# Kernel tuning notes

Measured on AMD Instinct MI355X. Metric: run time of the kernel, lower is better.

The kernel has to match this reference:

```python
import jax, jax.numpy as jnp
import numpy as np

ENTREG = 0.1          # blur passed to geomloss SamplesLoss
P_EXP = 2             # p=2 -> squared euclidean cost
EPS = ENTREG ** P_EXP # geomloss temperature eps = blur**p = 0.01
N_ITERS = 30          # fixed Sinkhorn iterations (geomloss tensorized loop)


def _squared_distances(x, y):
    # C[i,j] = ||x_i - y_j||^2  (geomloss.utils.squared_distances)
    x2 = jnp.sum(x * x, axis=-1)  # [n]
    y2 = jnp.sum(y * y, axis=-1)  # [m]
    return x2[:, None] + y2[None, :] - 2.0 * (x @ y.T)


def setup_inputs() -> dict:
    key = jax.random.key(0)
    k1, k2 = jax.random.split(key)
    Xs = jax.random.normal(k1, (4096, 1024), dtype=jnp.float32)
    Xt = jax.random.normal(k2, (4096, 1024), dtype=jnp.float32)
    return {"Xs": Xs, "Xt": Xt}


def _sinkhorn_plan(Xs, Xt):
    n, m = Xs.shape[0], Xt.shape[0]
    C = _squared_distances(Xs, Xt)          # [n, m]
    loga = -jnp.log(jnp.float32(n))         # uniform source weights (log)
    logb = -jnp.log(jnp.float32(m))         # uniform target weights (log)
    f0 = jnp.zeros((n,), dtype=C.dtype)
    g0 = jnp.zeros((m,), dtype=C.dtype)

    def step(carry, _):
        f, g = carry
        # softmin updates in log-domain (stable logsumexp), eps = blur**p
        g = -EPS * jax.nn.logsumexp((f[:, None] - C) / EPS + loga, axis=0)  # [m]
        f = -EPS * jax.nn.logsumexp((g[None, :] - C) / EPS + logb, axis=1)  # [n]
        return (f, g), None

    (f, g), _ = jax.lax.scan(jax.checkpoint(step), (f0, g0), None, length=N_ITERS)
    # closs: P = exp((u^T + v - C) / entreg)  -- note: entreg, not eps, as in source
    P = jnp.exp((f[:, None] + g[None, :] - C) / ENTREG)
    return P


def reference(Xs, Xt):
    return _sinkhorn_plan(Xs, Xt)
```

## Files before the change

### kernel.cpp

```cpp
#include <hip/hip_runtime.h>
#include <cstddef>
#include <cstdint>

#define N_PTS 4096
#define DIMK 1024

typedef _Float16 half8 __attribute__((ext_vector_type(8)));
typedef float floatx4 __attribute__((ext_vector_type(4)));

static constexpr float S_SCALE = 144.26950408889634f;
static constexpr float TWO_S   = 288.53900817779268f;
static constexpr float NEG_BIG = -3.4e38f;


__device__ __forceinline__ float4 f4max(float4 a, float4 b) {
  return make_float4(fmaxf(a.x, b.x), fmaxf(a.y, b.y), fmaxf(a.z, b.z), fmaxf(a.w, b.w));
}
__device__ __forceinline__ void msmerge(float4& M, float4& S, const float4 M2, const float4 S2) {
  float4 Mn = f4max(M, M2);
  S.x = S.x * exp2f(M.x - Mn.x) + S2.x * exp2f(M2.x - Mn.x);
  S.y = S.y * exp2f(M.y - Mn.y) + S2.y * exp2f(M2.y - Mn.y);
  S.z = S.z * exp2f(M.z - Mn.z) + S2.z * exp2f(M2.z - Mn.z);
  S.w = S.w * exp2f(M.w - Mn.w) + S2.w * exp2f(M2.w - Mn.w);
  M = Mn;
}

__global__ __launch_bounds__(256) void k_prep(const float* __restrict__ Xs,
                                              float* __restrict__ fvec) {
  int row  = blockIdx.x * 4 + (threadIdx.x >> 6);
  int lane = threadIdx.x & 63;
  const float* src = Xs + (size_t)row * DIMK;
  float s = 0.f;
#pragma unroll
  for (int r = 0; r < 4; ++r) {
    float4 a = *(const float4*)(src + lane * 4 + r * 256);
    s += a.x * a.x + a.y * a.y + a.z * a.z + a.w * a.w;
  }
#pragma unroll
  for (int off = 32; off; off >>= 1) s += __shfl_xor(s, off);
  if (lane == 0) fvec[row] = (1024.0f - s) * S_SCALE;
}

__global__ __launch_bounds__(256) void k_convert(const float* __restrict__ X,
                                                 _Float16* __restrict__ H,
                                                 _Float16* __restrict__ L) {
  size_t i8 = ((size_t)blockIdx.x * 256 + threadIdx.x) * 8;
  float4 a = *(const float4*)(X + i8);
  float4 b = *(const float4*)(X + i8 + 4);
  float v[8] = {a.x, a.y, a.z, a.w, b.x, b.y, b.z, b.w};
  half8 h, l;
#pragma unroll
  for (int q = 0; q < 8; ++q) {
    _Float16 hh = (_Float16)v[q];
    h[q] = hh;
    l[q] = (_Float16)(v[q] - (float)hh);
  }
  *(half8*)(H + i8) = h;
  *(half8*)(L + i8) = l;
}

__global__ __launch_bounds__(256) void k_gemm_mfma(const _Float16* __restrict__ Ah,
                                                   const _Float16* __restrict__ Al,
                                                   const _Float16* __restrict__ Bh,
                                                   const _Float16* __restrict__ Bl,
                                                   float* __restrict__ D,
                                                   float* __restrict__ DT) {
  __shared__ __align__(16) _Float16 Ahs[128 * 32];
  __shared__ __align__(16) _Float16 Als[128 * 32];
  __shared__ __align__(16) _Float16 Bhs[128 * 32];
  __shared__ __align__(16) _Float16 Bls[128 * 32];
  const int t    = threadIdx.x;
  const int lane = t & 63, wave = t >> 6;
  const int wm = wave >> 1, wn = wave & 1;
  const int lm = lane & 15, q = lane >> 4;
  const int row0 = blockIdx.y * 128, col0 = blockIdx.x * 128;

  floatx4 acc[4][4];
#pragma unroll
  for (int i = 0; i < 4; ++i)
#pragma unroll
    for (int j = 0; j < 4; ++j) acc[i][j] = (floatx4){0.f, 0.f, 0.f, 0.f};

  const int r0 = t >> 2, p0 = t & 3;
  const int r1 = 64 + r0;

  for (int k0 = 0; k0 < DIMK; k0 += 32) {
    size_t ga0 = (size_t)(row0 + r0) * DIMK + k0 + p0 * 8;
    size_t ga1 = (size_t)(row0 + r1) * DIMK + k0 + p0 * 8;
    size_t gb0 = (size_t)(col0 + r0) * DIMK + k0 + p0 * 8;
    size_t gb1 = (size_t)(col0 + r1) * DIMK + k0 + p0 * 8;
    half8 vah0 = *(const half8*)(Ah + ga0);
    half8 vah1 = *(const half8*)(Ah + ga1);
    half8 val0 = *(const half8*)(Al + ga0);
    half8 val1 = *(const half8*)(Al + ga1);
    half8 vbh0 = *(const half8*)(Bh + gb0);
    half8 vbh1 = *(const half8*)(Bh + gb1);
    half8 vbl0 = *(const half8*)(Bl + gb0);
    half8 vbl1 = *(const half8*)(Bl + gb1);
    __syncthreads();
    ((half8*)Ahs)[t] = vah0; ((half8*)Ahs)[t + 256] = vah1;
    ((half8*)Als)[t] = val0; ((half8*)Als)[t + 256] = val1;
    ((half8*)Bhs)[t] = vbh0; ((half8*)Bhs)[t + 256] = vbh1;
    ((half8*)Bls)[t] = vbl0; ((half8*)Bls)[t + 256] = vbl1;
    __syncthreads();

    half8 afh[4], afl[4], bfh[4], bfl[4];
#pragma unroll
    for (int i = 0; i < 4; ++i) {
      int ar = (wm * 64 + i * 16 + lm) * 32 + q * 8;
      int br = (wn * 64 + i * 16 + lm) * 32 + q * 8;
      afh[i] = *(const half8*)(Ahs + ar);
      afl[i] = *(const half8*)(Als + ar);
      bfh[i] = *(const half8*)(Bhs + br);
      bfl[i] = *(const half8*)(Bls + br);
    }
#pragma unroll
    for (int i = 0; i < 4; ++i)
#pragma unroll
      for (int j = 0; j < 4; ++j) {
        acc[i][j] = __builtin_amdgcn_mfma_f32_16x16x32_f16(afh[i], bfh[j], acc[i][j], 0, 0, 0);
        acc[i][j] = __builtin_amdgcn_mfma_f32_16x16x32_f16(afh[i], bfl[j], acc[i][j], 0, 0, 0);
        acc[i][j] = __builtin_amdgcn_mfma_f32_16x16x32_f16(afl[i], bfh[j], acc[i][j], 0, 0, 0);
      }
  }

#pragma unroll
  for (int i = 0; i < 4; ++i) {
    int mbase = row0 + wm * 64 + i * 16 + q * 4;
#pragma unroll
    for (int j = 0; j < 4; ++j) {
      int n = col0 + wn * 64 + j * 16 + lm;
      float vals[4];
#pragma unroll
      for (int r = 0; r < 4; ++r) {
        float vv = -TWO_S * acc[i][j][r];
        vals[r] = vv;
        D[(size_t)(mbase + r) * N_PTS + n] = vv;
      }
      if (DT) *(float4*)(DT + (size_t)n * N_PTS + mbase) = *(float4*)vals;
    }
  }
}

__global__ __launch_bounds__(256) void k_sweep2(const float* __restrict__ Mrow,
                                                const float* __restrict__ vin,
                                                float* __restrict__ vout) {
  __shared__ float vs[N_PTS];
  const int t = threadIdx.x;
  const int l = t & 63;
  const int row = blockIdx.x * 4 + (t >> 6);
#pragma unroll
  for (int k = 0; k < 4; ++k)
    *(float4*)(vs + t * 4 + k * 1024) = *(const float4*)(vin + t * 4 + k * 1024);
  __syncthreads();
  const float* rp_ = Mrow + (size_t)row * N_PTS;
  float4 dv[16];
#pragma unroll
  for (int k = 0; k < 16; ++k) dv[k] = *(const float4*)(rp_ + l * 4 + k * 256);
  float M = NEG_BIG, S = 0.f;
#pragma unroll
  for (int c = 0; c < 4; ++c) {
    float v[16];
#pragma unroll
    for (int q = 0; q < 4; ++q) {
      float4 d = dv[c * 4 + q];
      const float* gp = vs + l * 4 + (c * 4 + q) * 256;
      v[q * 4 + 0] = gp[0] - d.x; v[q * 4 + 1] = gp[1] - d.y;
      v[q * 4 + 2] = gp[2] - d.z; v[q * 4 + 3] = gp[3] - d.w;
    }
    float Mc = v[0];
#pragma unroll
    for (int q = 1; q < 16; ++q) Mc = fmaxf(Mc, v[q]);
    float Mn = fmaxf(M, Mc);
    float s = S * exp2f(M - Mn);
#pragma unroll
    for (int q = 0; q < 16; ++q) s += exp2f(v[q] - Mn);
    M = Mn; S = s;
  }
#pragma unroll
  for (int off = 32; off; off >>= 1) {
    float M2 = __shfl_xor(M, off);
    float S2 = __shfl_xor(S, off);
    float Mn = fmaxf(M, M2);
    S = S * exp2f(M - Mn) + S2 * exp2f(M2 - Mn);
    M = Mn;
  }
  if (l == 0) vout[row] = 12.0f - M - log2f(S);
}

__global__ __launch_bounds__(256) void k_sweepF(float* __restrict__ D,
                                                const float* __restrict__ gvec) {
  __shared__ float vs[N_PTS];
  const int t = threadIdx.x;
  const int l = t & 63;
  const int row = blockIdx.x * 4 + (t >> 6);
#pragma unroll
  for (int k = 0; k < 4; ++k)
    *(float4*)(vs + t * 4 + k * 1024) = *(const float4*)(gvec + t * 4 + k * 1024);
  __syncthreads();
  float* rp_ = D + (size_t)row * N_PTS;
  float4 dv[16];
#pragma unroll
  for (int k = 0; k < 16; ++k) dv[k] = *(const float4*)(rp_ + l * 4 + k * 256);
  float M = NEG_BIG, S = 0.f;
#pragma unroll
  for (int c = 0; c < 4; ++c) {
    float v[16];
#pragma unroll
    for (int q = 0; q < 4; ++q) {
      float4 d = dv[c * 4 + q];
      const float* gp = vs + l * 4 + (c * 4 + q) * 256;
      v[q * 4 + 0] = gp[0] - d.x; v[q * 4 + 1] = gp[1] - d.y;
      v[q * 4 + 2] = gp[2] - d.z; v[q * 4 + 3] = gp[3] - d.w;
    }
    float Mc = v[0];
#pragma unroll
    for (int q = 1; q < 16; ++q) Mc = fmaxf(Mc, v[q]);
    float Mn = fmaxf(M, Mc);
    float s = S * exp2f(M - Mn);
#pragma unroll
    for (int q = 0; q < 16; ++q) s += exp2f(v[q] - Mn);
    M = Mn; S = s;
  }
#pragma unroll
  for (int off = 32; off; off >>= 1) {
    float M2 = __shfl_xor(M, off);
    float S2 = __shfl_xor(S, off);
    float Mn = fmaxf(M, M2);
    S = S * exp2f(M - Mn) + S2 * exp2f(M2 - Mn);
    M = Mn;
  }
  const float fi = 12.0f - M - log2f(S);
#pragma unroll
  for (int k = 0; k < 16; ++k) {
    int j = l * 4 + k * 256;
    float4 d = dv[k];
    const float* gp = vs + j;
    d.x = exp2f(0.1f * (fi + gp[0] - d.x));
    d.y = exp2f(0.1f * (fi + gp[1] - d.y));
    d.z = exp2f(0.1f * (fi + gp[2] - d.z));
    d.w = exp2f(0.1f * (fi + gp[3] - d.w));
    *(float4*)(rp_ + j) = d;
  }
}

__device__ __forceinline__ float lse_row4096(const float* __restrict__ rowp,
                                             const float* __restrict__ vin,
                                             int l) {
  float4 dv[16], gv[16];
#pragma unroll
  for (int k = 0; k < 16; ++k) dv[k] = *(const float4*)(rowp + l * 4 + k * 256);
#pragma unroll
  for (int k = 0; k < 16; ++k) gv[k] = *(const float4*)(vin + l * 4 + k * 256);
  float M = NEG_BIG, S = 0.f;
#pragma unroll
  for (int c = 0; c < 4; ++c) {
    float v[16];
#pragma unroll
    for (int q = 0; q < 4; ++q) {
      float4 d = dv[c * 4 + q], g = gv[c * 4 + q];
      v[q * 4 + 0] = g.x - d.x; v[q * 4 + 1] = g.y - d.y;
      v[q * 4 + 2] = g.z - d.z; v[q * 4 + 3] = g.w - d.w;
    }
    float Mc = v[0];
#pragma unroll
    for (int q = 1; q < 16; ++q) Mc = fmaxf(Mc, v[q]);
    float Mn = fmaxf(M, Mc);
    float s = S * exp2f(M - Mn);
#pragma unroll
    for (int q = 0; q < 16; ++q) s += exp2f(v[q] - Mn);
    M = Mn; S = s;
  }
#pragma unroll
  for (int off = 32; off; off >>= 1) {
    float M2 = __shfl_xor(M, off);
    float S2 = __shfl_xor(S, off);
    float Mn = fmaxf(M, M2);
    S = S * exp2f(M - Mn) + S2 * exp2f(M2 - Mn);
    M = Mn;
  }
  return 12.0f - M - log2f(S);
}

__global__ __launch_bounds__(256) void k_sweep(const float* __restrict__ Mrow,
                                               const float* __restrict__ vin,
                                               float* __restrict__ vout) {
  const int l = threadIdx.x & 63;
  const int row = blockIdx.x * 4 + (threadIdx.x >> 6);
  float r = lse_row4096(Mrow + (size_t)row * N_PTS, vin, l);
  if (l == 0) vout[row] = r;
}

__global__ __launch_bounds__(1024) void k_colpass(const float* __restrict__ D,
                                                  const float* __restrict__ fvec,
                                                  float* __restrict__ gvec) {
  __shared__ float fs[N_PTS];
  __shared__ float4 MS[16][4][2];
  const int t = threadIdx.x;
  *(float4*)(fs + t * 4) = *(const float4*)(fvec + t * 4);
  __syncthreads();
  const int c4 = t & 3;
  const int rp = t >> 2;
  const float* base = D + blockIdx.x * 16 + c4 * 4;
  float4 M = make_float4(NEG_BIG, NEG_BIG, NEG_BIG, NEG_BIG);
  float4 S = make_float4(0.f, 0.f, 0.f, 0.f);
#pragma unroll
  for (int h = 0; h < 2; ++h) {
    float4 v[8];
#pragma unroll
    for (int qq = 0; qq < 8; ++qq) {
      int r = rp + (h * 8 + qq) * 256;
      float4 d = *(const float4*)(base + (size_t)r * N_PTS);
      float fr = fs[r];
      v[qq] = make_float4(fr - d.x, fr - d.y, fr - d.z, fr - d.w);
    }
    float4 Mc = f4max(f4max(f4max(v[0], v[1]), f4max(v[2], v[3])),
                      f4max(f4max(v[4], v[5]), f4max(v[6], v[7])));
    float4 Mn = f4max(M, Mc);
    float4 s;
    s.x = S.x * exp2f(M.x - Mn.x);
    s.y = S.y * exp2f(M.y - Mn.y);
    s.z = S.z * exp2f(M.z - Mn.z);
    s.w = S.w * exp2f(M.w - Mn.w);
#pragma unroll
    for (int qq = 0; qq < 8; ++qq) {
      s.x += exp2f(v[qq].x - Mn.x);
      s.y += exp2f(v[qq].y - Mn.y);
      s.z += exp2f(v[qq].z - Mn.z);
      s.w += exp2f(v[qq].w - Mn.w);
    }
    M = Mn; S = s;
  }
#pragma unroll
  for (int off = 4; off <= 32; off <<= 1) {
    float4 M2, S2;
    M2.x = __shfl_xor(M.x, off); M2.y = __shfl_xor(M.y, off);
    M2.z = __shfl_xor(M.z, off); M2.w = __shfl_xor(M.w, off);
    S2.x = __shfl_xor(S.x, off); S2.y = __shfl_xor(S.y, off);
    S2.z = __shfl_xor(S.z, off); S2.w = __shfl_xor(S.w, off);
    msmerge(M, S, M2, S2);
  }
  const int wv = t >> 6, l = t & 63;
  if (l < 4) { MS[wv][l][0] = M; MS[wv][l][1] = S; }
  __syncthreads();
  if (t < 4) {
    float4 M0 = MS[0][t][0], S0 = MS[0][t][1];
#pragma unroll
    for (int w = 1; w < 16; ++w) msmerge(M0, S0, MS[w][t][0], MS[w][t][1]);
    float4 g;
    g.x = 12.0f - M0.x - log2f(S0.x);
    g.y = 12.0f - M0.y - log2f(S0.y);
    g.z = 12.0f - M0.z - log2f(S0.z);
    g.w = 12.0f - M0.w - log2f(S0.w);
    *(float4*)(gvec + blockIdx.x * 16 + t * 4) = g;
  }
}

__global__ __launch_bounds__(256) void k_final(float* __restrict__ D,
                                               const float* __restrict__ fvec,
                                               const float* __restrict__ gvec) {
  size_t idx = ((size_t)blockIdx.x * 256 + threadIdx.x) * 8;
  int i = (int)(idx >> 12);
  int j = (int)(idx & (N_PTS - 1));
  float fi = fvec[i];
#pragma unroll
  for (int h = 0; h < 2; ++h) {
    float4 d  = *(float4*)(D + idx + h * 4);
    float4 g4 = *(const float4*)(gvec + j + h * 4);
    d.x = exp2f(0.1f * (fi + g4.x - d.x));
    d.y = exp2f(0.1f * (fi + g4.y - d.y));
    d.z = exp2f(0.1f * (fi + g4.z - d.z));
    d.w = exp2f(0.1f * (fi + g4.w - d.w));
    *(float4*)(D + idx + h * 4) = d;
  }
}

__global__ __launch_bounds__(256) void k_gemm(const float* __restrict__ A,
                                              const float* __restrict__ B,
                                              float* __restrict__ D) {
  __shared__ float As[16][132];
  __shared__ float Bs[16][132];
  const int t  = threadIdx.x;
  const int tx = t & 15, ty = t >> 4;
  const int row0 = blockIdx.y * 128, col0 = blockIdx.x * 128;
  float acc[8][8];
#pragma unroll
  for (int i = 0; i < 8; ++i)
#pragma unroll
    for (int j = 0; j < 8; ++j) acc[i][j] = 0.f;
  for (int k0 = 0; k0 < DIMK; k0 += 16) {
#pragma unroll
    for (int s2 = 0; s2 < 2; ++s2) {
      int f4i = t + s2 * 256;
      int r   = f4i >> 2;
      int kp  = (f4i & 3) << 2;
      float4 a4 = *(const float4*)(A + (size_t)(row0 + r) * DIMK + k0 + kp);
      float4 b4 = *(const float4*)(B + (size_t)(col0 + r) * DIMK + k0 + kp);
      As[kp + 0][r] = a4.x; As[kp + 1][r] = a4.y; As[kp + 2][r] = a4.z; As[kp + 3][r] = a4.w;
      Bs[kp + 0][r] = b4.x; Bs[kp + 1][r] = b4.y; Bs[kp + 2][r] = b4.z; Bs[kp + 3][r] = b4.w;
    }
    __syncthreads();
#pragma unroll
    for (int kk = 0; kk < 16; ++kk) {
      float a[8], b[8];
      *(float4*)(a)     = *(const float4*)(&As[kk][ty * 4]);
      *(float4*)(a + 4) = *(const float4*)(&As[kk][64 + ty * 4]);
      *(float4*)(b)     = *(const float4*)(&Bs[kk][tx * 4]);
      *(float4*)(b + 4) = *(const float4*)(&Bs[kk][64 + tx * 4]);
#pragma unroll
      for (int i = 0; i < 8; ++i)
#pragma unroll
        for (int j = 0; j < 8; ++j) acc[i][j] = fmaf(a[i], b[j], acc[i][j]);
    }
    __syncthreads();
  }
#pragma unroll
  for (int i = 0; i < 8; ++i) {
    int r = row0 + ((i < 4) ? (ty * 4 + i) : (64 + ty * 4 + (i - 4)));
    float* out = D + (size_t)r * N_PTS + col0;
    float4 o1, o2;
    o1.x = -TWO_S * acc[i][0]; o1.y = -TWO_S * acc[i][1];
    o1.z = -TWO_S * acc[i][2]; o1.w = -TWO_S * acc[i][3];
    o2.x = -TWO_S * acc[i][4]; o2.y = -TWO_S * acc[i][5];
    o2.z = -TWO_S * acc[i][6]; o2.w = -TWO_S * acc[i][7];
    *(float4*)(out + tx * 4)      = o1;
    *(float4*)(out + 64 + tx * 4) = o2;
  }
}

extern "C" void kernel_launch(void* const* d_in, const int* in_sizes, int n_in,
                              void* d_out, int out_size, void* d_ws, size_t ws_size,
                              hipStream_t stream) {
  const float* Xs = (const float*)d_in[0];
  const float* Xt = (const float*)d_in[1];
  float* D   = (float*)d_out;
  char* wsb  = (char*)d_ws;
  float* fvec = (float*)wsb;
  float* gvec = fvec + N_PTS;

  const size_t halfElems = (size_t)N_PTS * DIMK;
  const size_t offHalves = 32768;
  _Float16* Ah = (_Float16*)(wsb + offHalves);
  _Float16* Al = Ah + halfElems;
  _Float16* Bh = Al + halfElems;
  _Float16* Bl = Bh + halfElems;
  float* DT = (float*)(wsb + offHalves + 4 * halfElems * sizeof(_Float16));
  const size_t needHalves = offHalves + 4 * halfElems * sizeof(_Float16);
  const size_t needFull   = needHalves + (size_t)N_PTS * N_PTS * sizeof(float);
  const bool haveH = ws_size >= needHalves;
  const bool haveT = ws_size >= needFull;

  k_prep<<<1024, 256, 0, stream>>>(Xs, fvec);
  if (haveH) {
    k_convert<<<2048, 256, 0, stream>>>(Xs, Ah, Al);
    k_convert<<<2048, 256, 0, stream>>>(Xt, Bh, Bl);
    k_gemm_mfma<<<dim3(32, 32), 256, 0, stream>>>(Ah, Al, Bh, Bl, D, haveT ? DT : nullptr);
  } else {
    k_gemm<<<dim3(32, 32), 256, 0, stream>>>(Xs, Xt, D);
  }

  if (haveT) {
    for (int it = 0; it < 30; ++it) {
      k_sweep2<<<1024, 256, 0, stream>>>(DT, fvec, gvec);
      if (it < 29) k_sweep2<<<1024, 256, 0, stream>>>(D, gvec, fvec);
      else         k_sweepF<<<1024, 256, 0, stream>>>(D, gvec);
    }
  } else {
    for (int it = 0; it < 30; ++it) {
      k_colpass<<<256, 1024, 0, stream>>>(D, fvec, gvec);
      k_sweep<<<1024, 256, 0, stream>>>(D, gvec, fvec);
    }
    k_final<<<8192, 256, 0, stream>>>(D, fvec, gvec);
  }
}
```

Measured before the change: 989.3 us.

## Fuse row and column Sinkhorn passes into one sweep with partial column merges

Drops the transposed copy of the cost matrix and the separate column sweep. Each iteration now reads the matrix once: a fused kernel computes the row logsumexp to update f, then accumulates per-block online column max/sum partials, and a small merge kernel reduces 256 partials into g. This halves the matrix traffic per iteration and avoids writing a 64MB transpose in the GEMM epilogue. In exchange it adds a __syncthreads per row inside the fused kernel, only 256 blocks of parallelism, and an extra launch plus partial-buffer traffic per iteration.

```diff
diff --git a/kernel.cpp b/kernel.cpp
--- a/kernel.cpp
+++ b/kernel.cpp
@@ -4,6 +4,7 @@
 
 #define N_PTS 4096
 #define DIMK 1024
+#define N_PART 256
 
 typedef _Float16 half8 __attribute__((ext_vector_type(8)));
 typedef float floatx4 __attribute__((ext_vector_type(4)));
@@ -63,8 +64,7 @@
                                                    const _Float16* __restrict__ Al,
                                                    const _Float16* __restrict__ Bh,
                                                    const _Float16* __restrict__ Bl,
-                                                   float* __restrict__ D,
-                                                   float* __restrict__ DT) {
+                                                   float* __restrict__ D) {
   __shared__ __align__(16) _Float16 Ahs[128 * 32];
   __shared__ __align__(16) _Float16 Als[128 * 32];
   __shared__ __align__(16) _Float16 Bhs[128 * 32];
@@ -130,62 +130,133 @@
 #pragma unroll
     for (int j = 0; j < 4; ++j) {
       int n = col0 + wn * 64 + j * 16 + lm;
-      float vals[4];
-#pragma unroll
-      for (int r = 0; r < 4; ++r) {
-        float vv = -TWO_S * acc[i][j][r];
-        vals[r] = vv;
-        D[(size_t)(mbase + r) * N_PTS + n] = vv;
+#pragma unroll
+      for (int r = 0; r < 4; ++r)
+        D[(size_t)(mbase + r) * N_PTS + n] = -TWO_S * acc[i][j][r];
+    }
+  }
+}
+
+__global__ __launch_bounds__(512) void k_fused(const float* __restrict__ D,
+                                               float* __restrict__ fvec,
+                                               const float* __restrict__ gv,
+                                               float* __restrict__ PM,
+                                               float* __restrict__ PS,
+                                               int do_row) {
+  __shared__ float gs[N_PTS];
+  __shared__ float MS[2][8][2];
+  const int t = threadIdx.x;
+  const int l = t & 63, w = t >> 6;
+  const int col0 = w * 512;
+  const int r0 = blockIdx.x * 16;
+  if (do_row) {
+#pragma unroll
+    for (int k = 0; k < 2; ++k)
+      *(float4*)(gs + t * 4 + k * 2048) = *(const float4*)(gv + t * 4 + k * 2048);
+    __syncthreads();
+  }
+  float4 aM[2], aS[2];
+#pragma unroll
+  for (int k = 0; k < 2; ++k) {
+    aM[k] = make_float4(NEG_BIG, NEG_BIG, NEG_BIG, NEG_BIG);
+    aS[k] = make_float4(0.f, 0.f, 0.f, 0.f);
+  }
+  for (int rr = 0; rr < 16; ++rr) {
+    const int row = r0 + rr;
+    const float* rp = D + (size_t)row * N_PTS + col0;
+    float4 dv[2];
+#pragma unroll
+    for (int k = 0; k < 2; ++k) dv[k] = *(const float4*)(rp + l * 4 + k * 256);
+    float fi;
+    if (do_row) {
+      float v[8];
+#pragma unroll
+      for (int k = 0; k < 2; ++k) {
+        const float* gp = gs + col0 + l * 4 + k * 256;
+        v[k * 4 + 0] = gp[0] - dv[k].x; v[k * 4 + 1] = gp[1] - dv[k].y;
+        v[k * 4 + 2] = gp[2] - dv[k].z; v[k * 4 + 3] = gp[3] - dv[k].w;
       }
-      if (DT) *(float4*)(DT + (size_t)n * N_PTS + mbase) = *(float4*)vals;
-    }
-  }
-}
-
-__global__ __launch_bounds__(256) void k_sweep2(const float* __restrict__ Mrow,
-                                                const float* __restrict__ vin,
-                                                float* __restrict__ vout) {
-  __shared__ float vs[N_PTS];
+      float M = v[0];
+#pragma unroll
+      for (int q = 1; q < 8; ++q) M = fmaxf(M, v[q]);
+      float S = 0.f;
+#pragma unroll
+      for (int q = 0; q < 8; ++q) S += exp2f(v[q] - M);
+#pragma unroll
+      for (int off = 32; off; off >>= 1) {
+        float M2 = __shfl_xor(M, off), S2 = __shfl_xor(S, off);
+        float Mn = fmaxf(M, M2);
+        S = S * exp2f(M - Mn) + S2 * exp2f(M2 - Mn);
+        M = Mn;
+      }
+      if (l == 0) { MS[rr & 1][w][0] = M; MS[rr & 1][w][1] = S; }
+      __syncthreads();
+      float Mb = MS[rr & 1][0][0], Sb = MS[rr & 1][0][1];
+#pragma unroll
+      for (int p = 1; p < 8; ++p) {
+        float M1 = MS[rr & 1][p][0], S1 = MS[rr & 1][p][1];
+        float Mn = fmaxf(Mb, M1);
+        Sb = Sb * exp2f(Mb - Mn) + S1 * exp2f(M1 - Mn);
+        Mb = Mn;
+      }
+      fi = 12.0f - Mb - log2f(Sb);
+      if (t == 0) fvec[row] = fi;
+    } else {
+      fi = fvec[row];
+    }
+#pragma unroll
+    for (int k = 0; k < 2; ++k) {
+      float* mp = (float*)&aM[k];
+      float* sp = (float*)&aS[k];
+      const float* dp = (const float*)&dv[k];
+#pragma unroll
+      for (int c = 0; c < 4; ++c) {
+        float vv = fi - dp[c];
+        float d  = vv - mp[c];
+        float e  = exp2f(-fabsf(d));
+        bool  gt = d > 0.f;
+        sp[c] = gt ? fmaf(sp[c], e, 1.0f) : (sp[c] + e);
+        mp[c] = gt ? vv : mp[c];
+      }
+    }
+  }
+  float* pmb = PM + (size_t)blockIdx.x * N_PTS + col0;
+  float* psb = PS + (size_t)blockIdx.x * N_PTS + col0;
+#pragma unroll
+  for (int k = 0; k < 2; ++k) {
+    *(float4*)(pmb + l * 4 + k * 256) = aM[k];
+    *(float4*)(psb + l * 4 + k * 256) = aS[k];
+  }
+}
+
+__global__ __launch_bounds__(256) void k_cmerge(const float* __restrict__ PM,
+                                                const float* __restrict__ PS,
+                                                float* __restrict__ gvec) {
   const int t = threadIdx.x;
-  const int l = t & 63;
-  const int row = blockIdx.x * 4 + (t >> 6);
-#pragma unroll
-  for (int k = 0; k < 4; ++k)
-    *(float4*)(vs + t * 4 + k * 1024) = *(const float4*)(vin + t * 4 + k * 1024);
+  const int c = blockIdx.x * 32 + (t & 31);
+  const int q = t >> 5;
+  float M = NEG_BIG, S = 0.f;
+#pragma unroll 4
+  for (int p = q * 32; p < q * 32 + 32; ++p) {
+    float M1 = PM[(size_t)p * N_PTS + c];
+    float S1 = PS[(size_t)p * N_PTS + c];
+    float Mn = fmaxf(M, M1);
+    S = S * exp2f(M - Mn) + S1 * exp2f(M1 - Mn);
+    M = Mn;
+  }
+  __shared__ float LM[8][32], LS[8][32];
+  LM[q][t & 31] = M; LS[q][t & 31] = S;
   __syncthreads();
-  const float* rp_ = Mrow + (size_t)row * N_PTS;
-  float4 dv[16];
-#pragma unroll
-  for (int k = 0; k < 16; ++k) dv[k] = *(const float4*)(rp_ + l * 4 + k * 256);
-  float M = NEG_BIG, S = 0.f;
-#pragma unroll
-  for (int c = 0; c < 4; ++c) {
-    float v[16];
-#pragma unroll
-    for (int q = 0; q < 4; ++q) {
-      float4 d = dv[c * 4 + q];
-      const float* gp = vs + l * 4 + (c * 4 + q) * 256;
-      v[q * 4 + 0] = gp[0] - d.x; v[q * 4 + 1] = gp[1] - d.y;
-      v[q * 4 + 2] = gp[2] - d.z; v[q * 4 + 3] = gp[3] - d.w;
-    }
-    float Mc = v[0];
-#pragma unroll
-    for (int q = 1; q < 16; ++q) Mc = fmaxf(Mc, v[q]);
-    float Mn = fmaxf(M, Mc);
-    float s = S * exp2f(M - Mn);
-#pragma unroll
-    for (int q = 0; q < 16; ++q) s += exp2f(v[q] - Mn);
-    M = Mn; S = s;
-  }
-#pragma unroll
-  for (int off = 32; off; off >>= 1) {
-    float M2 = __shfl_xor(M, off);
-    float S2 = __shfl_xor(S, off);
-    float Mn = fmaxf(M, M2);
-    S = S * exp2f(M - Mn) + S2 * exp2f(M2 - Mn);
-    M = Mn;
-  }
-  if (l == 0) vout[row] = 12.0f - M - log2f(S);
+  if (q == 0) {
+#pragma unroll
+    for (int p = 1; p < 8; ++p) {
+      float M1 = LM[p][t], S1 = LS[p][t];
+      float Mn = fmaxf(M, M1);
+      S = S * exp2f(M - Mn) + S1 * exp2f(M1 - Mn);
+      M = Mn;
+    }
+    gvec[c] = 12.0f - M - log2f(S);
+  }
 }
 
 __global__ __launch_bounds__(256) void k_sweepF(float* __restrict__ D,
@@ -295,7 +366,7 @@
                                                   const float* __restrict__ fvec,
                                                   float* __restrict__ gvec) {
   __shared__ float fs[N_PTS];
-  __shared__ float4 MS[16][4][2];
+  __shared__ float4 MSx[16][4][2];
   const int t = threadIdx.x;
   *(float4*)(fs + t * 4) = *(const float4*)(fvec + t * 4);
   __syncthreads();
@@ -341,12 +412,12 @@
     msmerge(M, S, M2, S2);
   }
   const int wv = t >> 6, l = t & 63;
-  if (l < 4) { MS[wv][l][0] = M; MS[wv][l][1] = S; }
+  if (l < 4) { MSx[wv][l][0] = M; MSx[wv][l][1] = S; }
   __syncthreads();
   if (t < 4) {
-    float4 M0 = MS[0][t][0], S0 = MS[0][t][1];
-#pragma unroll
-    for (int w = 1; w < 16; ++w) msmerge(M0, S0, MS[w][t][0], MS[w][t][1]);
+    float4 M0 = MSx[0][t][0], S0 = MSx[0][t][1];
+#pragma unroll
+    for (int w = 1; w < 16; ++w) msmerge(M0, S0, MSx[w][t][0], MSx[w][t][1]);
     float4 g;
     g.x = 12.0f - M0.x - log2f(S0.x);
     g.y = 12.0f - M0.y - log2f(S0.y);
@@ -444,9 +515,10 @@
   _Float16* Al = Ah + halfElems;
   _Float16* Bh = Al + halfElems;
   _Float16* Bl = Bh + halfElems;
-  float* DT = (float*)(wsb + offHalves + 4 * halfElems * sizeof(_Float16));
+  float* PM = (float*)(wsb + offHalves + 4 * halfElems * sizeof(_Float16));
+  float* PS = PM + (size_t)N_PART * N_PTS;
   const size_t needHalves = offHalves + 4 * halfElems * sizeof(_Float16);
-  const size_t needFull   = needHalves + (size_t)N_PTS * N_PTS * sizeof(float);
+  const size_t needFull   = needHalves + 2 * (size_t)N_PART * N_PTS * sizeof(float);
   const bool haveH = ws_size >= needHalves;
   const bool haveT = ws_size >= needFull;
 
@@ -454,17 +526,19 @@
   if (haveH) {
     k_convert<<<2048, 256, 0, stream>>>(Xs, Ah, Al);
     k_convert<<<2048, 256, 0, stream>>>(Xt, Bh, Bl);
-    k_gemm_mfma<<<dim3(32, 32), 256, 0, stream>>>(Ah, Al, Bh, Bl, D, haveT ? DT : nullptr);
+    k_gemm_mfma<<<dim3(32, 32), 256, 0, stream>>>(Ah, Al, Bh, Bl, D);
   } else {
     k_gemm<<<dim3(32, 32), 256, 0, stream>>>(Xs, Xt, D);
   }
 
   if (haveT) {
-    for (int it = 0; it < 30; ++it) {
-      k_sweep2<<<1024, 256, 0, stream>>>(DT, fvec, gvec);
-      if (it < 29) k_sweep2<<<1024, 256, 0, stream>>>(D, gvec, fvec);
-      else         k_sweepF<<<1024, 256, 0, stream>>>(D, gvec);
-    }
+    k_fused<<<N_PART, 512, 0, stream>>>(D, fvec, gvec, PM, PS, 0);
+    k_cmerge<<<128, 256, 0, stream>>>(PM, PS, gvec);
+    for (int it = 1; it < 30; ++it) {
+      k_fused<<<N_PART, 512, 0, stream>>>(D, fvec, gvec, PM, PS, 1);
+      k_cmerge<<<128, 256, 0, stream>>>(PM, PS, gvec);
+    }
+    k_sweepF<<<1024, 256, 0, stream>>>(D, gvec);
   } else {
     for (int it = 0; it < 30; ++it) {
       k_colpass<<<256, 1024, 0, stream>>>(D, fvec, gvec);
```

Result: slower. 1.467 ms (+48.3%).
